# Optimization experiments

Hardware: AMD Instinct MI355X
Metric: run time of the kernel (lower is better)

## Reference

```python
import jax, jax.numpy as jnp
import numpy as np

B, S, D = 2, 2048, 1024
QH, KVH, DH = 16, 4, 64
TOP_K = 128
ROPE_BASE = 10000.0


def _rope(x):
    # x: [B, H, S, DH]; standard LLaMA-style rotate-half RoPE, no freq scaling
    half = DH // 2
    inv_freq = 1.0 / (ROPE_BASE ** (jnp.arange(half, dtype=jnp.float32) / half))
    ang = jnp.arange(S, dtype=jnp.float32)[:, None] * inv_freq[None, :]  # [S, half]
    cos, sin = jnp.cos(ang), jnp.sin(ang)
    x1, x2 = x[..., :half], x[..., half:]
    return jnp.concatenate([x1 * cos - x2 * sin, x2 * cos + x1 * sin], axis=-1)


def setup_inputs() -> dict:
    key = jax.random.key(0)
    ks = jax.random.split(key, 5)
    return {
        "x": jax.random.normal(ks[0], (B, S, D), dtype=jnp.float32),
        "Wq": jax.random.normal(ks[1], (QH * DH, D), dtype=jnp.float32) * 0.02,
        "Wk": jax.random.normal(ks[2], (KVH * DH, D), dtype=jnp.float32) * 0.02,
        "Wv": jax.random.normal(ks[3], (KVH * DH, D), dtype=jnp.float32) * 0.02,
        "Wo": jax.random.normal(ks[4], (D, QH * DH), dtype=jnp.float32) * 0.02,
    }


def reference(x, Wq, Wk, Wv, Wo):
    # projections (Linear, no bias): y = x @ W.T
    q = (x @ Wq.T).reshape(B, S, QH, DH).transpose(0, 2, 1, 3)   # [B,QH,S,DH]
    k = (x @ Wk.T).reshape(B, S, KVH, DH).transpose(0, 2, 1, 3)  # [B,KVH,S,DH]
    v = (x @ Wv.T).reshape(B, S, KVH, DH).transpose(0, 2, 1, 3)
    q = _rope(q)
    k = _rope(k)
    # repeat_kv: GQA expand kv heads to q heads
    rep = QH // KVH
    k = jnp.repeat(k, rep, axis=1)
    v = jnp.repeat(v, rep, axis=1)
    scores = jnp.einsum("bhqd,bhkd->bhqk", q, k) / np.sqrt(DH)  # [B,QH,S,S]
    causal = jnp.triu(jnp.ones((S, S), dtype=bool), k=1)
    scores = jnp.where(causal, -jnp.inf, scores)
    # top-k masking before softmax: keep entries >= per-row k-th largest score
    top_vals = jax.lax.top_k(scores, TOP_K)[0]        # [B,QH,S,TOP_K]
    thr = top_vals[..., -1:]
    scores = jnp.where(scores < thr, -jnp.inf, scores)
    w = jax.nn.softmax(scores, axis=-1)
    out = jnp.einsum("bhqk,bhkd->bhqd", w, v)         # [B,QH,S,DH]
    out = out.transpose(0, 2, 1, 3).reshape(B, S, QH * DH)
    return out @ Wo.T
```

## Files before the change

### kernel.cpp

```cpp
#include <hip/hip_runtime.h>
#include <hip/hip_bf16.h>
#include <hip/hip_fp16.h>
#include <math.h>

constexpr int cB   = 2;
constexpr int cS   = 2048;
constexpr int cD   = 1024;
constexpr int cQH  = 16;
constexpr int cKVH = 4;
constexpr int cDH  = 64;
constexpr int cTOPK = 128;
constexpr int cM   = cB * cS;
constexpr int cNB  = cS / 64;
constexpr int cLSZ = 384;

constexpr int cTI  = 8;
constexpr int cSTR = 130;

typedef __attribute__((ext_vector_type(8))) short short8;
typedef __attribute__((ext_vector_type(4))) float floatx4;
typedef _Float16 half8 __attribute__((ext_vector_type(8)));

__device__ inline ushort f2bf(float f) {
    unsigned u = __float_as_uint(f);
    return (ushort)((u + 0x7FFFu + ((u >> 16) & 1u)) >> 16);
}

__global__ void cast_f32_bf16(const float* __restrict__ src,
                              ushort* __restrict__ dst, int n) {
    int i4 = (blockIdx.x * blockDim.x + threadIdx.x) * 4;
    if (i4 >= n) return;
    const float4 v = *(const float4*)(src + i4);
    ushort4 r;
    r.x = f2bf(v.x); r.y = f2bf(v.y); r.z = f2bf(v.z); r.w = f2bf(v.w);
    *(ushort4*)(dst + i4) = r;
}

__global__ void cast_f32_f16(const float* __restrict__ src,
                             ushort* __restrict__ dst, int n) {
    int i4 = (blockIdx.x * blockDim.x + threadIdx.x) * 4;
    if (i4 >= n) return;
    const float4 v = *(const float4*)(src + i4);
    ushort4 r;
    r.x = __builtin_bit_cast(ushort, (_Float16)v.x);
    r.y = __builtin_bit_cast(ushort, (_Float16)v.y);
    r.z = __builtin_bit_cast(ushort, (_Float16)v.z);
    r.w = __builtin_bit_cast(ushort, (_Float16)v.w);
    *(ushort4*)(dst + i4) = r;
}

__global__ __launch_bounds__(256) void gemm_bf16_bt(
        const ushort* __restrict__ A, const ushort* __restrict__ W,
        float* __restrict__ C, int M, int N, int K) {
    __shared__ short As[4][128][8];
    __shared__ short Bs[4][128][8];

    const int tid  = threadIdx.x;
    const int lane = tid & 63;
    const int w    = tid >> 6;
    const int wm   = (w & 1) * 64;
    const int wn   = (w >> 1) * 64;
    const int m0   = blockIdx.y * 128;
    const int n0   = blockIdx.x * 128;

    const int quad = lane >> 4;
    const int l16  = lane & 15;

    floatx4 acc[4][4];
    #pragma unroll
    for (int mi = 0; mi < 4; ++mi)
        #pragma unroll
        for (int ni = 0; ni < 4; ++ni)
            acc[mi][ni] = (floatx4){0.f, 0.f, 0.f, 0.f};

    const int sr = tid >> 1;
    const int sh = (tid & 1) * 2;

    for (int k0 = 0; k0 < K; k0 += 32) {
        const ushort* sa = A + (size_t)(m0 + sr) * K + k0 + sh * 8;
        const short8 a0 = *(const short8*)sa;
        const short8 a1 = *(const short8*)(sa + 8);
        const ushort* sw = W + (size_t)(n0 + sr) * K + k0 + sh * 8;
        const short8 b0 = *(const short8*)sw;
        const short8 b1 = *(const short8*)(sw + 8);
        *(short8*)&As[sh][sr][0]     = a0;
        *(short8*)&As[sh + 1][sr][0] = a1;
        *(short8*)&Bs[sh][sr][0]     = b0;
        *(short8*)&Bs[sh + 1][sr][0] = b1;
        __syncthreads();

        short8 af[4], bf[4];
        #pragma unroll
        for (int mi = 0; mi < 4; ++mi)
            af[mi] = *(const short8*)&As[quad][wm + mi * 16 + l16][0];
        #pragma unroll
        for (int ni = 0; ni < 4; ++ni)
            bf[ni] = *(const short8*)&Bs[quad][wn + ni * 16 + l16][0];
        #pragma unroll
        for (int mi = 0; mi < 4; ++mi)
            #pragma unroll
            for (int ni = 0; ni < 4; ++ni)
                acc[mi][ni] = __builtin_amdgcn_mfma_f32_16x16x32_bf16(
                    af[mi], bf[ni], acc[mi][ni], 0, 0, 0);
        __syncthreads();
    }

    #pragma unroll
    for (int mi = 0; mi < 4; ++mi)
        #pragma unroll
        for (int ni = 0; ni < 4; ++ni)
            #pragma unroll
            for (int r = 0; r < 4; ++r) {
                const int row = m0 + wm + mi * 16 + quad * 4 + r;
                const int col = n0 + wn + ni * 16 + l16;
                C[(size_t)row * N + col] = acc[mi][ni][r];
            }
}

__global__ void rope_cast_f16(const float* __restrict__ src,
                              ushort* __restrict__ dst, int H, int total,
                              float scale) {
    int idx = blockIdx.x * blockDim.x + threadIdx.x;
    if (idx >= total) return;
    const int d   = idx & 31;
    const int h   = (idx >> 5) % H;
    const int row = idx / (32 * H);
    const int s   = row % cS;
    const float inv_freq = powf(10000.0f, -(float)d / 32.0f);
    const float ang = (float)s * inv_freq;
    const float c  = cosf(ang);
    const float si = sinf(ang);
    const float* p = src + (size_t)row * H * cDH + (size_t)h * cDH;
    const float x1 = p[d];
    const float x2 = p[d + 32];
    const float r1 = (x1 * c - x2 * si) * scale;
    const float r2 = (x2 * c + x1 * si) * scale;
    ushort* o = dst + (size_t)row * H * cDH + (size_t)h * cDH;
    o[d]      = __builtin_bit_cast(ushort, (_Float16)r1);
    o[d + 32] = __builtin_bit_cast(ushort, (_Float16)r2);
}

__device__ inline unsigned fmap(float f) {
    unsigned u = __float_as_uint(f);
    return (u & 0x80000000u) ? ~u : (u | 0x80000000u);
}
__device__ inline float funmap(unsigned u) {
    unsigned v = (u & 0x80000000u) ? (u & 0x7FFFFFFFu) : ~u;
    return __uint_as_float(v);
}

__global__ __launch_bounds__(512) void attn_tile_kernel(
        const ushort* __restrict__ qf, const ushort* __restrict__ kf,
        const ushort* __restrict__ vf, ushort* __restrict__ out) {
    extern __shared__ char smem[];
    unsigned* stg = (unsigned*)smem;
    unsigned* klA = (unsigned*)smem;
    int*      jlA = (int*)(klA + cTI * cLSZ);

    const int lane = threadIdx.x & 63;
    const int wv   = __builtin_amdgcn_readfirstlane(threadIdx.x >> 6);

    const int x  = blockIdx.x;
    const int it = (cS / cTI - 1) - (x >> 5);
    const int bh = x & 31;
    const int h  = bh & 15;
    const int b  = bh >> 4;
    const int kvh = h >> 2;
    const int i0  = it * cTI;

    const size_t bS = (size_t)b * cS;
    const int l16   = lane & 15;
    const int quad  = lane >> 4;
    const int jperm = ((lane & 3) << 4) + (lane >> 2);
    const int i     = i0 + wv;

    const ushort* qp = qf + ((bS + i0 + (l16 & 7)) * cQH + h) * cDH + quad * 8;
    const half8 a0h = __builtin_bit_cast(half8, *(const uint4*)qp);
    const half8 a1h = __builtin_bit_cast(half8, *(const uint4*)(qp + 32));

    unsigned key[cNB];
    #pragma unroll
    for (int jb = 0; jb < cNB; ++jb) key[jb] = 0u;

    const int nk16   = ((i0 + cTI - 1) >> 4) + 1;
    const int nchunk = (nk16 + 7) >> 3;

    #pragma unroll
    for (int c = 0; c < 16; ++c) {
        if (c >= nchunk) break;
        const int  kb16  = (c << 3) + wv;
        if (kb16 < nk16) {
            const ushort* kp = kf + ((bS + (kb16 << 4) + l16) * cKVH + kvh) * cDH + quad * 8;
            const uint4 b0 = *(const uint4*)kp;
            const uint4 b1 = *(const uint4*)(kp + 32);
            floatx4 acc = (floatx4){0.f, 0.f, 0.f, 0.f};
            acc = __builtin_amdgcn_mfma_f32_16x16x32_f16(
                a0h, __builtin_bit_cast(half8, b0), acc, 0, 0, 0);
            acc = __builtin_amdgcn_mfma_f32_16x16x32_f16(
                a1h, __builtin_bit_cast(half8, b1), acc, 0, 0, 0);
            if (quad < 2) {
                const int jg = (kb16 << 4) + l16;
                unsigned* sp = stg + (c & 1) * (cTI * cSTR) + (wv << 4) + l16;
                #pragma unroll
                for (int r2 = 0; r2 < 4; ++r2) {
                    const int qrow = quad * 4 + r2;
                    sp[qrow * cSTR] = (jg <= i0 + qrow) ? fmap(acc[r2]) : 0u;
                }
            }
        }
        __syncthreads();
        {
            const unsigned* rp = stg + (c & 1) * (cTI * cSTR) + wv * cSTR;
            #pragma unroll
            for (int jj = 0; jj < 2; ++jj) {
                const int j = (c << 7) + (jj << 6) + jperm;
                const unsigned kr = rp[(jj << 6) + jperm];
                key[(c << 1) + jj] = (j <= i) ? kr : 0u;
            }
        }
    }
    __syncthreads();

    const int nb = (i >> 6) + 1;
    unsigned* kl = klA + wv * cLSZ;
    int*      jl = jlA + wv * cLSZ;
    const int vbase0 = (int)(((unsigned)bS * cKVH + kvh) * cDH);

    unsigned um = 0u, un = 0xFFFFFFFFu;
    #pragma unroll
    for (int jb = 0; jb < cNB; ++jb) {
        if (jb >= nb) break;
        const unsigned kk = key[jb];
        um = max(um, kk);
        un = min(un, kk ? kk : 0xFFFFFFFFu);
    }
    #pragma unroll
    for (int off = 32; off >= 1; off >>= 1) {
        um = max(um, (unsigned)__shfl_xor((int)um, off));
        un = min(un, (unsigned)__shfl_xor((int)un, off));
    }
    const float mrow = funmap(um);

    unsigned ustar;
    if (i < cTOPK) {
        ustar = un;
    } else {
        unsigned lo = un, hi = um;
        while (lo < hi) {
            const unsigned d   = hi - lo;
            const unsigned mid = lo + (d >> 1) + (d & 1u);
            int cnt2 = 0;
            #pragma unroll
            for (int jb = 0; jb < cNB; ++jb) {
                if (jb >= nb) break;
                cnt2 += __popcll(__ballot(key[jb] >= mid));
            }
            if (cnt2 == cTOPK) {
                unsigned mn = 0xFFFFFFFFu;
                #pragma unroll
                for (int jb = 0; jb < cNB; ++jb) {
                    if (jb >= nb) break;
                    const unsigned kk = key[jb];
                    mn = min(mn, (kk >= mid) ? kk : 0xFFFFFFFFu);
                }
                #pragma unroll
                for (int off = 32; off >= 1; off >>= 1)
                    mn = min(mn, (unsigned)__shfl_xor((int)mn, off));
                lo = mn;
                break;
            }
            if (cnt2 > cTOPK) lo = mid; else hi = mid - 1u;
        }
        ustar = lo;
    }

    const unsigned long long mlt = (1ull << lane) - 1ull;
    int base = 0;
    #pragma unroll
    for (int jb = 0; jb < cNB; ++jb) {
        if (jb >= nb) break;
        const int j = (jb << 6) + jperm;
        const bool keep = (j <= i) && (key[jb] >= ustar);
        const unsigned long long mk = __ballot(keep);
        const int pos = base + __popcll(mk & mlt);
        if (keep && pos < cLSZ) {
            kl[pos] = key[jb];
            jl[pos] = vbase0 + j * (cKVH * cDH);
        }
        base += __popcll(mk);
    }
    const int cnt = min(base, cLSZ);

    float zp = 0.f;
    for (int t = lane; t < cnt; t += 64) {
        const float s  = funmap(kl[t]);
        const float wt = __expf(s - mrow);
        ((float*)kl)[t] = wt;
        zp += wt;
    }
    #pragma unroll
    for (int off = 32; off >= 1; off >>= 1) zp += __shfl_xor(zp, off);
    const float invZ = 1.0f / zp;

    float ac0 = 0.f, ac1 = 0.f, ac2 = 0.f, ac3 = 0.f;
    float ac4 = 0.f, ac5 = 0.f, ac6 = 0.f, ac7 = 0.f;
    int t = 0;
    #pragma unroll 2
    for (; t + 7 < cnt; t += 8) {
        const float wt0 = ((float*)kl)[t];
        const float wt1 = ((float*)kl)[t + 1];
        const float wt2 = ((float*)kl)[t + 2];
        const float wt3 = ((float*)kl)[t + 3];
        const float wt4 = ((float*)kl)[t + 4];
        const float wt5 = ((float*)kl)[t + 5];
        const float wt6 = ((float*)kl)[t + 6];
        const float wt7 = ((float*)kl)[t + 7];
        const int vo0 = jl[t];
        const int vo1 = jl[t + 1];
        const int vo2 = jl[t + 2];
        const int vo3 = jl[t + 3];
        const int vo4 = jl[t + 4];
        const int vo5 = jl[t + 5];
        const int vo6 = jl[t + 6];
        const int vo7 = jl[t + 7];
        ac0 += wt0 * (float)__builtin_bit_cast(_Float16, vf[vo0 + lane]);
        ac1 += wt1 * (float)__builtin_bit_cast(_Float16, vf[vo1 + lane]);
        ac2 += wt2 * (float)__builtin_bit_cast(_Float16, vf[vo2 + lane]);
        ac3 += wt3 * (float)__builtin_bit_cast(_Float16, vf[vo3 + lane]);
        ac4 += wt4 * (float)__builtin_bit_cast(_Float16, vf[vo4 + lane]);
        ac5 += wt5 * (float)__builtin_bit_cast(_Float16, vf[vo5 + lane]);
        ac6 += wt6 * (float)__builtin_bit_cast(_Float16, vf[vo6 + lane]);
        ac7 += wt7 * (float)__builtin_bit_cast(_Float16, vf[vo7 + lane]);
    }
    for (; t < cnt; ++t) {
        const float wt = ((float*)kl)[t];
        const int   vo = jl[t];
        ac0 += wt * (float)__builtin_bit_cast(_Float16, vf[vo + lane]);
    }
    const float acc = ((ac0 + ac1) + (ac2 + ac3)) + ((ac4 + ac5) + (ac6 + ac7));
    out[((bS + i) * cQH + h) * cDH + lane] = f2bf(acc * invZ);
}

extern "C" void kernel_launch(void* const* d_in, const int* in_sizes, int n_in,
                              void* d_out, int out_size, void* d_ws, size_t ws_size,
                              hipStream_t stream) {
    const float* x  = (const float*)d_in[0];
    const float* Wq = (const float*)d_in[1];
    const float* Wk = (const float*)d_in[2];
    const float* Wv = (const float*)d_in[3];
    const float* Wo = (const float*)d_in[4];
    float* out = (float*)d_out;

    float* ws = (float*)d_ws;
    float*  qb  = ws;
    float*  kb  = qb + (size_t)cM * cQH * cDH;
    float*  vb  = kb + (size_t)cM * cKVH * cDH;
    ushort* xh  = (ushort*)(vb + (size_t)cM * cKVH * cDH);
    ushort* Wqh = xh  + (size_t)cM * cD;
    ushort* Wkh = Wqh + (size_t)cQH * cDH * cD;
    ushort* Wvh = Wkh + (size_t)cKVH * cDH * cD;
    ushort* Woh = Wvh + (size_t)cKVH * cDH * cD;
    ushort* abh = Woh + (size_t)cD * cQH * cDH;
    ushort* kff = abh + (size_t)cM * cQH * cDH;
    ushort* qff = kff + (size_t)cM * cKVH * cDH;
    ushort* vff = (ushort*)kb;

    dim3 blk(256);

    {
        const int nx  = cM * cD;
        const int nwq = cQH * cDH * cD;
        const int nwk = cKVH * cDH * cD;
        const int nwo = cD * cQH * cDH;
        cast_f32_bf16<<<(nx / 4 + 255) / 256, blk, 0, stream>>>(x, xh, nx);
        cast_f32_bf16<<<(nwq / 4 + 255) / 256, blk, 0, stream>>>(Wq, Wqh, nwq);
        cast_f32_bf16<<<(nwk / 4 + 255) / 256, blk, 0, stream>>>(Wk, Wkh, nwk);
        cast_f32_bf16<<<(nwk / 4 + 255) / 256, blk, 0, stream>>>(Wv, Wvh, nwk);
        cast_f32_bf16<<<(nwo / 4 + 255) / 256, blk, 0, stream>>>(Wo, Woh, nwo);
    }

    gemm_bf16_bt<<<dim3((cQH * cDH) / 128, cM / 128), blk, 0, stream>>>(xh, Wqh, qb, cM, cQH * cDH, cD);
    gemm_bf16_bt<<<dim3((cKVH * cDH) / 128, cM / 128), blk, 0, stream>>>(xh, Wkh, kb, cM, cKVH * cDH, cD);
    gemm_bf16_bt<<<dim3((cKVH * cDH) / 128, cM / 128), blk, 0, stream>>>(xh, Wvh, vb, cM, cKVH * cDH, cD);

    {
        int totq = cM * cQH * 32;
        int totk = cM * cKVH * 32;
        rope_cast_f16<<<(totq + 255) / 256, blk, 0, stream>>>(qb, qff, cQH, totq, 0.125f);
        rope_cast_f16<<<(totk + 255) / 256, blk, 0, stream>>>(kb, kff, cKVH, totk, 1.0f);
        const int nv = cM * cKVH * cDH;
        cast_f32_f16<<<(nv / 4 + 255) / 256, blk, 0, stream>>>(vb, vff, nv);
    }

    constexpr size_t aSMEM = (size_t)cTI * cLSZ * 8;
    static_assert(2 * cTI * cSTR * 4 <= (int)aSMEM, "staging must fit");
    attn_tile_kernel<<<dim3(32 * (cS / cTI)), dim3(512), aSMEM, stream>>>(
        qff, kff, vff, abh);

    gemm_bf16_bt<<<dim3(cD / 128, cM / 128), blk, 0, stream>>>(abh, Woh, out, cM, cD, cD);
}
```

Baseline: 588.0 us.

## Fuse RoPE and f16 casts into projection GEMM epilogues; scalarize V gather offsets

```diff
diff --git a/kernel.cpp b/kernel.cpp
--- a/kernel.cpp
+++ b/kernel.cpp
@@ -33,19 +33,6 @@
     const float4 v = *(const float4*)(src + i4);
     ushort4 r;
     r.x = f2bf(v.x); r.y = f2bf(v.y); r.z = f2bf(v.z); r.w = f2bf(v.w);
-    *(ushort4*)(dst + i4) = r;
-}
-
-__global__ void cast_f32_f16(const float* __restrict__ src,
-                             ushort* __restrict__ dst, int n) {
-    int i4 = (blockIdx.x * blockDim.x + threadIdx.x) * 4;
-    if (i4 >= n) return;
-    const float4 v = *(const float4*)(src + i4);
-    ushort4 r;
-    r.x = __builtin_bit_cast(ushort, (_Float16)v.x);
-    r.y = __builtin_bit_cast(ushort, (_Float16)v.y);
-    r.z = __builtin_bit_cast(ushort, (_Float16)v.z);
-    r.w = __builtin_bit_cast(ushort, (_Float16)v.w);
     *(ushort4*)(dst + i4) = r;
 }
 
@@ -117,27 +104,154 @@
             }
 }
 
-__global__ void rope_cast_f16(const float* __restrict__ src,
-                              ushort* __restrict__ dst, int H, int total,
-                              float scale) {
-    int idx = blockIdx.x * blockDim.x + threadIdx.x;
-    if (idx >= total) return;
-    const int d   = idx & 31;
-    const int h   = (idx >> 5) % H;
-    const int row = idx / (32 * H);
-    const int s   = row % cS;
-    const float inv_freq = powf(10000.0f, -(float)d / 32.0f);
-    const float ang = (float)s * inv_freq;
-    const float c  = cosf(ang);
-    const float si = sinf(ang);
-    const float* p = src + (size_t)row * H * cDH + (size_t)h * cDH;
-    const float x1 = p[d];
-    const float x2 = p[d + 32];
-    const float r1 = (x1 * c - x2 * si) * scale;
-    const float r2 = (x2 * c + x1 * si) * scale;
-    ushort* o = dst + (size_t)row * H * cDH + (size_t)h * cDH;
-    o[d]      = __builtin_bit_cast(ushort, (_Float16)r1);
-    o[d + 32] = __builtin_bit_cast(ushort, (_Float16)r2);
+__global__ __launch_bounds__(256) void gemm_bf16_bt_rope_f16(
+        const ushort* __restrict__ A, const ushort* __restrict__ W,
+        ushort* __restrict__ C, int M, int N, int K, float scale) {
+    __shared__ short As[4][128][8];
+    __shared__ short Bs[4][128][8];
+
+    const int tid  = threadIdx.x;
+    const int lane = tid & 63;
+    const int w    = tid >> 6;
+    const int wm   = (w & 1) * 64;
+    const int wn   = (w >> 1) * 64;
+    const int m0   = blockIdx.y * 128;
+    const int n0   = blockIdx.x * 128;
+
+    const int quad = lane >> 4;
+    const int l16  = lane & 15;
+
+    floatx4 acc[4][4];
+    #pragma unroll
+    for (int mi = 0; mi < 4; ++mi)
+        #pragma unroll
+        for (int ni = 0; ni < 4; ++ni)
+            acc[mi][ni] = (floatx4){0.f, 0.f, 0.f, 0.f};
+
+    const int sr = tid >> 1;
+    const int sh = (tid & 1) * 2;
+
+    for (int k0 = 0; k0 < K; k0 += 32) {
+        const ushort* sa = A + (size_t)(m0 + sr) * K + k0 + sh * 8;
+        const short8 a0 = *(const short8*)sa;
+        const short8 a1 = *(const short8*)(sa + 8);
+        const ushort* sw = W + (size_t)(n0 + sr) * K + k0 + sh * 8;
+        const short8 b0 = *(const short8*)sw;
+        const short8 b1 = *(const short8*)(sw + 8);
+        *(short8*)&As[sh][sr][0]     = a0;
+        *(short8*)&As[sh + 1][sr][0] = a1;
+        *(short8*)&Bs[sh][sr][0]     = b0;
+        *(short8*)&Bs[sh + 1][sr][0] = b1;
+        __syncthreads();
+
+        short8 af[4], bf[4];
+        #pragma unroll
+        for (int mi = 0; mi < 4; ++mi)
+            af[mi] = *(const short8*)&As[quad][wm + mi * 16 + l16][0];
+        #pragma unroll
+        for (int ni = 0; ni < 4; ++ni)
+            bf[ni] = *(const short8*)&Bs[quad][wn + ni * 16 + l16][0];
+        #pragma unroll
+        for (int mi = 0; mi < 4; ++mi)
+            #pragma unroll
+            for (int ni = 0; ni < 4; ++ni)
+                acc[mi][ni] = __builtin_amdgcn_mfma_f32_16x16x32_bf16(
+                    af[mi], bf[ni], acc[mi][ni], 0, 0, 0);
+        __syncthreads();
+    }
+
+    #pragma unroll
+    for (int ni = 0; ni < 2; ++ni) {
+        const int colL = n0 + wn + ni * 16 + l16;
+        const int d    = colL & 31;
+        const float inv_freq = powf(10000.0f, -(float)d / 32.0f);
+        #pragma unroll
+        for (int mi = 0; mi < 4; ++mi)
+            #pragma unroll
+            for (int r = 0; r < 4; ++r) {
+                const int row = m0 + wm + mi * 16 + quad * 4 + r;
+                const int s   = row & (cS - 1);
+                const float ang = (float)s * inv_freq;
+                const float c   = cosf(ang);
+                const float si  = sinf(ang);
+                const float x1  = acc[mi][ni][r];
+                const float x2  = acc[mi][ni + 2][r];
+                const float r1  = (x1 * c - x2 * si) * scale;
+                const float r2  = (x2 * c + x1 * si) * scale;
+                ushort* o = C + (size_t)row * N + colL;
+                o[0]  = __builtin_bit_cast(ushort, (_Float16)r1);
+                o[32] = __builtin_bit_cast(ushort, (_Float16)r2);
+            }
+    }
+}
+
+__global__ __launch_bounds__(256) void gemm_bf16_bt_f16(
+        const ushort* __restrict__ A, const ushort* __restrict__ W,
+        ushort* __restrict__ C, int M, int N, int K) {
+    __shared__ short As[4][128][8];
+    __shared__ short Bs[4][128][8];
+
+    const int tid  = threadIdx.x;
+    const int lane = tid & 63;
+    const int w    = tid >> 6;
+    const int wm   = (w & 1) * 64;
+    const int wn   = (w >> 1) * 64;
+    const int m0   = blockIdx.y * 128;
+    const int n0   = blockIdx.x * 128;
+
+    const int quad = lane >> 4;
+    const int l16  = lane & 15;
+
+    floatx4 acc[4][4];
+    #pragma unroll
+    for (int mi = 0; mi < 4; ++mi)
+        #pragma unroll
+        for (int ni = 0; ni < 4; ++ni)
+            acc[mi][ni] = (floatx4){0.f, 0.f, 0.f, 0.f};
+
+    const int sr = tid >> 1;
+    const int sh = (tid & 1) * 2;
+
+    for (int k0 = 0; k0 < K; k0 += 32) {
+        const ushort* sa = A + (size_t)(m0 + sr) * K + k0 + sh * 8;
+        const short8 a0 = *(const short8*)sa;
+        const short8 a1 = *(const short8*)(sa + 8);
+        const ushort* sw = W + (size_t)(n0 + sr) * K + k0 + sh * 8;
+        const short8 b0 = *(const short8*)sw;
+        const short8 b1 = *(const short8*)(sw + 8);
+        *(short8*)&As[sh][sr][0]     = a0;
+        *(short8*)&As[sh + 1][sr][0] = a1;
+        *(short8*)&Bs[sh][sr][0]     = b0;
+        *(short8*)&Bs[sh + 1][sr][0] = b1;
+        __syncthreads();
+
+        short8 af[4], bf[4];
+        #pragma unroll
+        for (int mi = 0; mi < 4; ++mi)
+            af[mi] = *(const short8*)&As[quad][wm + mi * 16 + l16][0];
+        #pragma unroll
+        for (int ni = 0; ni < 4; ++ni)
+            bf[ni] = *(const short8*)&Bs[quad][wn + ni * 16 + l16][0];
+        #pragma unroll
+        for (int mi = 0; mi < 4; ++mi)
+            #pragma unroll
+            for (int ni = 0; ni < 4; ++ni)
+                acc[mi][ni] = __builtin_amdgcn_mfma_f32_16x16x32_bf16(
+                    af[mi], bf[ni], acc[mi][ni], 0, 0, 0);
+        __syncthreads();
+    }
+
+    #pragma unroll
+    for (int mi = 0; mi < 4; ++mi)
+        #pragma unroll
+        for (int ni = 0; ni < 4; ++ni)
+            #pragma unroll
+            for (int r = 0; r < 4; ++r) {
+                const int row = m0 + wm + mi * 16 + quad * 4 + r;
+                const int col = n0 + wn + ni * 16 + l16;
+                C[(size_t)row * N + col] =
+                    __builtin_bit_cast(ushort, (_Float16)acc[mi][ni][r]);
+            }
 }
 
 __device__ inline unsigned fmap(float f) {
@@ -149,7 +263,9 @@
     return __uint_as_float(v);
 }
 
-__global__ __launch_bounds__(512) void attn_tile_kernel(
+__global__ __launch_bounds__(512)
+__attribute__((amdgpu_waves_per_eu(4, 8)))
+void attn_tile_kernel(
         const ushort* __restrict__ qf, const ushort* __restrict__ kf,
         const ushort* __restrict__ vf, ushort* __restrict__ out) {
     extern __shared__ char smem[];
@@ -315,27 +431,27 @@
         const float wt5 = ((float*)kl)[t + 5];
         const float wt6 = ((float*)kl)[t + 6];
         const float wt7 = ((float*)kl)[t + 7];
-        const int vo0 = jl[t];
-        const int vo1 = jl[t + 1];
-        const int vo2 = jl[t + 2];
-        const int vo3 = jl[t + 3];
-        const int vo4 = jl[t + 4];
-        const int vo5 = jl[t + 5];
-        const int vo6 = jl[t + 6];
-        const int vo7 = jl[t + 7];
-        ac0 += wt0 * (float)__builtin_bit_cast(_Float16, vf[vo0 + lane]);
-        ac1 += wt1 * (float)__builtin_bit_cast(_Float16, vf[vo1 + lane]);
-        ac2 += wt2 * (float)__builtin_bit_cast(_Float16, vf[vo2 + lane]);
-        ac3 += wt3 * (float)__builtin_bit_cast(_Float16, vf[vo3 + lane]);
-        ac4 += wt4 * (float)__builtin_bit_cast(_Float16, vf[vo4 + lane]);
-        ac5 += wt5 * (float)__builtin_bit_cast(_Float16, vf[vo5 + lane]);
-        ac6 += wt6 * (float)__builtin_bit_cast(_Float16, vf[vo6 + lane]);
-        ac7 += wt7 * (float)__builtin_bit_cast(_Float16, vf[vo7 + lane]);
+        const int so0 = __builtin_amdgcn_readfirstlane(jl[t]);
+        const int so1 = __builtin_amdgcn_readfirstlane(jl[t + 1]);
+        const int so2 = __builtin_amdgcn_readfirstlane(jl[t + 2]);
+        const int so3 = __builtin_amdgcn_readfirstlane(jl[t + 3]);
+        const int so4 = __builtin_amdgcn_readfirstlane(jl[t + 4]);
+        const int so5 = __builtin_amdgcn_readfirstlane(jl[t + 5]);
+        const int so6 = __builtin_amdgcn_readfirstlane(jl[t + 6]);
+        const int so7 = __builtin_amdgcn_readfirstlane(jl[t + 7]);
+        ac0 += wt0 * (float)__builtin_bit_cast(_Float16, vf[so0 + lane]);
+        ac1 += wt1 * (float)__builtin_bit_cast(_Float16, vf[so1 + lane]);
+        ac2 += wt2 * (float)__builtin_bit_cast(_Float16, vf[so2 + lane]);
+        ac3 += wt3 * (float)__builtin_bit_cast(_Float16, vf[so3 + lane]);
+        ac4 += wt4 * (float)__builtin_bit_cast(_Float16, vf[so4 + lane]);
+        ac5 += wt5 * (float)__builtin_bit_cast(_Float16, vf[so5 + lane]);
+        ac6 += wt6 * (float)__builtin_bit_cast(_Float16, vf[so6 + lane]);
+        ac7 += wt7 * (float)__builtin_bit_cast(_Float16, vf[so7 + lane]);
     }
     for (; t < cnt; ++t) {
         const float wt = ((float*)kl)[t];
-        const int   vo = jl[t];
-        ac0 += wt * (float)__builtin_bit_cast(_Float16, vf[vo + lane]);
+        const int   so = __builtin_amdgcn_readfirstlane(jl[t]);
+        ac0 += wt * (float)__builtin_bit_cast(_Float16, vf[so + lane]);
     }
     const float acc = ((ac0 + ac1) + (ac2 + ac3)) + ((ac4 + ac5) + (ac6 + ac7));
     out[((bS + i) * cQH + h) * cDH + lane] = f2bf(acc * invZ);
@@ -351,19 +467,15 @@
     const float* Wo = (const float*)d_in[4];
     float* out = (float*)d_out;
 
-    float* ws = (float*)d_ws;
-    float*  qb  = ws;
-    float*  kb  = qb + (size_t)cM * cQH * cDH;
-    float*  vb  = kb + (size_t)cM * cKVH * cDH;
-    ushort* xh  = (ushort*)(vb + (size_t)cM * cKVH * cDH);
+    ushort* xh  = (ushort*)d_ws;
     ushort* Wqh = xh  + (size_t)cM * cD;
     ushort* Wkh = Wqh + (size_t)cQH * cDH * cD;
     ushort* Wvh = Wkh + (size_t)cKVH * cDH * cD;
     ushort* Woh = Wvh + (size_t)cKVH * cDH * cD;
     ushort* abh = Woh + (size_t)cD * cQH * cDH;
-    ushort* kff = abh + (size_t)cM * cQH * cDH;
-    ushort* qff = kff + (size_t)cM * cKVH * cDH;
-    ushort* vff = (ushort*)kb;
+    ushort* qff = abh + (size_t)cM * cQH * cDH;
+    ushort* kff = qff + (size_t)cM * cQH * cDH;
+    ushort* vff = kff + (size_t)cM * cKVH * cDH;
 
     dim3 blk(256);
 
@@ -379,18 +491,12 @@
         cast_f32_bf16<<<(nwo / 4 + 255) / 256, blk, 0, stream>>>(Wo, Woh, nwo);
     }
 
-    gemm_bf16_bt<<<dim3((cQH * cDH) / 128, cM / 128), blk, 0, stream>>>(xh, Wqh, qb, cM, cQH * cDH, cD);
-    gemm_bf16_bt<<<dim3((cKVH * cDH) / 128, cM / 128), blk, 0, stream>>>(xh, Wkh, kb, cM, cKVH * cDH, cD);
-    gemm_bf16_bt<<<dim3((cKVH * cDH) / 128, cM / 128), blk, 0, stream>>>(xh, Wvh, vb, cM, cKVH * cDH, cD);
-
-    {
-        int totq = cM * cQH * 32;
-        int totk = cM * cKVH * 32;
-        rope_cast_f16<<<(totq + 255) / 256, blk, 0, stream>>>(qb, qff, cQH, totq, 0.125f);
-        rope_cast_f16<<<(totk + 255) / 256, blk, 0, stream>>>(kb, kff, cKVH, totk, 1.0f);
-        const int nv = cM * cKVH * cDH;
-        cast_f32_f16<<<(nv / 4 + 255) / 256, blk, 0, stream>>>(vb, vff, nv);
-    }
+    gemm_bf16_bt_rope_f16<<<dim3((cQH * cDH) / 128, cM / 128), blk, 0, stream>>>(
+        xh, Wqh, qff, cM, cQH * cDH, cD, 0.125f);
+    gemm_bf16_bt_rope_f16<<<dim3((cKVH * cDH) / 128, cM / 128), blk, 0, stream>>>(
+        xh, Wkh, kff, cM, cKVH * cDH, cD, 1.0f);
+    gemm_bf16_bt_f16<<<dim3((cKVH * cDH) / 128, cM / 128), blk, 0, stream>>>(
+        xh, Wvh, vff, cM, cKVH * cDH, cD);
 
     constexpr size_t aSMEM = (size_t)cTI * cLSZ * 8;
     static_assert(2 * cTI * cSTR * 4 <= (int)aSMEM, "staging must fit");
```

New measurement: 701.6 us. 1.19x slower.
